# Kernel optimization log

Hardware: AMD Instinct MI355X
Metric: run time of the kernel (lower is better)

Reference implementation:

```python
import jax, jax.numpy as jnp
import numpy as np

NUM_HEADS = 8
NUM_KEY_FEATURES = 128  # 32*1 + 32*3 (key fiber num_features)
N_NODES = 50000
N_EDGES = 500000
CH = 32  # value/key channels per degree


def setup_inputs() -> dict:
    key = jax.random.key(0)
    ks = jax.random.split(key, 7)
    return {
        "key0": jax.random.normal(ks[0], (N_EDGES, CH, 1), jnp.float32),
        "key1": jax.random.normal(ks[1], (N_EDGES, CH, 3), jnp.float32),
        "value0": jax.random.normal(ks[2], (N_EDGES, CH, 1), jnp.float32),
        "value1": jax.random.normal(ks[3], (N_EDGES, CH, 3), jnp.float32),
        "query0": jax.random.normal(ks[4], (N_NODES, CH, 1), jnp.float32),
        "query1": jax.random.normal(ks[5], (N_NODES, CH, 3), jnp.float32),
        "dst": jax.random.randint(ks[6], (N_EDGES,), 0, N_NODES, jnp.int64),
    }


def _to_heads(d0, d1):
    # Fiber.to_attention_heads: per-degree [*, C, 2d+1] -> [*, H, C//H*(2d+1)], concat over degrees
    a = d0.reshape(d0.shape[0], NUM_HEADS, -1)
    b = d1.reshape(d1.shape[0], NUM_HEADS, -1)
    return jnp.concatenate([a, b], axis=-1)  # [*, H, 16]


def reference(key0, key1, value0, value1, query0, query1, dst):
    n_nodes = query0.shape[0]
    k = _to_heads(key0, key1)      # [E, H, F]
    q = _to_heads(query0, query1)  # [N, H, F]
    # dgl.ops.e_dot_v: dot(key_e, query_{dst(e)}) per head
    logits = jnp.einsum('ehf,ehf->eh', k, q[dst]) / np.sqrt(NUM_KEY_FEATURES).astype(np.float32)
    # edge_softmax over incoming edges of each dst node
    m = jax.ops.segment_max(logits, dst, num_segments=n_nodes)       # [N, H]
    ex = jnp.exp(logits - m[dst])                                    # [E, H]
    s = jax.ops.segment_sum(ex, dst, num_segments=n_nodes)          # [N, H]
    w = ex / s[dst]                                                  # [E, H]

    def agg(v):
        e, c, dd = v.shape
        vh = v.reshape(e, NUM_HEADS, c // NUM_HEADS, dd)
        wv = w[:, :, None, None] * vh                                # [E, H, C/H, 2d+1]
        out = jax.ops.segment_sum(wv, dst, num_segments=n_nodes)
        return out.reshape(n_nodes, c, dd)                           # [N, C, 2d+1]

    return agg(value0), agg(value1)
```

## Files before the change

kernel.cpp:

```cpp
#include <hip/hip_runtime.h>
#include <hip/hip_bf16.h>
#include <math.h>

#define NHEADS 8
#define CHVAL 32
#define SCB 1024
#define WPB 4

__global__ void logits_kernel(const float4* __restrict__ key0,
                              const float4* __restrict__ key1,
                              const float4* __restrict__ q0,
                              const float4* __restrict__ q1,
                              const int* __restrict__ dst,
                              float* __restrict__ logits,
                              int* __restrict__ cnt,
                              int EH) {
    int tid = blockIdx.x * blockDim.x + threadIdx.x;
    if (tid >= EH) return;
    int e = tid >> 3;
    int h = tid & 7;
    int n = dst[e];
    int qh = n * 8 + h;

    float4 a = key0[tid];
    float4 qa = q0[qh];
    float dot = a.x * qa.x + a.y * qa.y + a.z * qa.z + a.w * qa.w;
#pragma unroll
    for (int j = 0; j < 3; ++j) {
        float4 b  = key1[tid * 3 + j];
        float4 qb = q1[qh * 3 + j];
        dot += b.x * qb.x + b.y * qb.y + b.z * qb.z + b.w * qb.w;
    }
    logits[tid] = dot * 0.08838834764831845f;
    if (h == 0) atomicAdd(&cnt[n], 1);
}

__global__ void scan1_kernel(int* __restrict__ cnt, int* __restrict__ btot, int N) {
    __shared__ int sh[SCB];
    int t = threadIdx.x;
    int i = blockIdx.x * SCB + t;
    int v = (i < N) ? cnt[i] : 0;
    sh[t] = v;
    __syncthreads();
    for (int off = 1; off < SCB; off <<= 1) {
        int y = (t >= off) ? sh[t - off] : 0;
        __syncthreads();
        sh[t] += y;
        __syncthreads();
    }
    if (i < N) cnt[i] = sh[t] - v;
    if (t == SCB - 1) btot[blockIdx.x] = sh[t];
}

__global__ void scan2_kernel(int* __restrict__ btot, int nb) {
    __shared__ int sh[64];
    int t = threadIdx.x;
    int v = (t < nb) ? btot[t] : 0;
    sh[t] = v;
    __syncthreads();
    for (int off = 1; off < 64; off <<= 1) {
        int y = (t >= off) ? sh[t - off] : 0;
        __syncthreads();
        sh[t] += y;
        __syncthreads();
    }
    if (t < nb) btot[t] = sh[t] - v;
}

__global__ void scan3_kernel(const int* __restrict__ cnt, const int* __restrict__ btot,
                             int* __restrict__ offs, int* __restrict__ cursor,
                             int N, int E) {
    int i = blockIdx.x * blockDim.x + threadIdx.x;
    if (i < N) {
        int o = cnt[i] + btot[i >> 10];
        offs[i] = o;
        cursor[i] = o;
    }
    if (i == 0) offs[N] = E;
}

__global__ void scatter_kernel(const int* __restrict__ dst,
                               int* __restrict__ cursor,
                               int* __restrict__ eid,
                               int E) {
    int e = blockIdx.x * blockDim.x + threadIdx.x;
    if (e < E) {
        int pos = atomicAdd(&cursor[dst[e]], 1);
        eid[pos] = e;
    }
}

__global__ void __launch_bounds__(64 * WPB)
node_kernel(const float* __restrict__ logits,
            const float4* __restrict__ value0,
            const float4* __restrict__ value1,
            const int* __restrict__ offs,
            const int* __restrict__ eid,
            float4* __restrict__ out0,
            float4* __restrict__ out1,
            int N) {
    __shared__ float w_sh[WPB][64][9];

    int wv = threadIdx.x >> 6;
    int t  = threadIdx.x & 63;
    int n  = blockIdx.x * WPB + wv;
    if (n >= N) return;

    int beg = offs[n];
    int deg = offs[n + 1] - beg;

    if (deg == 0) {
        float4 z = {0.f, 0.f, 0.f, 0.f};
        if (t < 8) out0[(size_t)n * 8 + t] = z;
        else if (t < 32) out1[(size_t)n * 24 + (t - 8)] = z;
        return;
    }

    int myeid = -1;
    float lg[8];
    if (t < deg) {
        myeid = eid[beg + t];
        const float4* lp = (const float4*)(logits + (size_t)myeid * 8);
        float4 a = lp[0], b = lp[1];
        lg[0] = a.x; lg[1] = a.y; lg[2] = a.z; lg[3] = a.w;
        lg[4] = b.x; lg[5] = b.y; lg[6] = b.z; lg[7] = b.w;
    } else {
#pragma unroll
        for (int k = 0; k < 8; ++k) lg[k] = -INFINITY;
    }

    float mx[8];
#pragma unroll
    for (int k = 0; k < 8; ++k) mx[k] = lg[k];
    for (int base = 64; base < deg; base += 64) {
        if (base + t < deg) {
            int e = eid[beg + base + t];
            const float4* lp = (const float4*)(logits + (size_t)e * 8);
            float4 a = lp[0], b = lp[1];
            float tt[8] = {a.x, a.y, a.z, a.w, b.x, b.y, b.z, b.w};
#pragma unroll
            for (int k = 0; k < 8; ++k) mx[k] = fmaxf(mx[k], tt[k]);
        }
    }
#pragma unroll
    for (int k = 0; k < 8; ++k)
        for (int off = 32; off; off >>= 1)
            mx[k] = fmaxf(mx[k], __shfl_xor(mx[k], off, 64));

    float ex0[8], sm[8];
#pragma unroll
    for (int k = 0; k < 8; ++k) { ex0[k] = __expf(lg[k] - mx[k]); sm[k] = ex0[k]; }
    for (int base = 64; base < deg; base += 64) {
        if (base + t < deg) {
            int e = eid[beg + base + t];
            const float4* lp = (const float4*)(logits + (size_t)e * 8);
            float4 a = lp[0], b = lp[1];
            float tt[8] = {a.x, a.y, a.z, a.w, b.x, b.y, b.z, b.w};
#pragma unroll
            for (int k = 0; k < 8; ++k) sm[k] += __expf(tt[k] - mx[k]);
        }
    }
#pragma unroll
    for (int k = 0; k < 8; ++k)
        for (int off = 32; off; off >>= 1)
            sm[k] += __shfl_xor(sm[k], off, 64);
    float inv[8];
#pragma unroll
    for (int k = 0; k < 8; ++k) inv[k] = 1.0f / sm[k];

    int half = t >> 5;
    int l = t & 31;
    int myh = (l < 8) ? l : ((l - 8) / 3);
    float4 acc = {0.f, 0.f, 0.f, 0.f};

    for (int base = 0; base < deg; base += 64) {
        int clen = min(64, deg - base);
        if (base == 0) {
            if (t < clen) {
#pragma unroll
                for (int k = 0; k < 8; ++k) w_sh[wv][t][k] = ex0[k] * inv[k];
            }
        } else {
            if (base + t < deg) {
                int e = eid[beg + base + t];
                const float4* lp = (const float4*)(logits + (size_t)e * 8);
                float4 a = lp[0], b = lp[1];
                float tt[8] = {a.x, a.y, a.z, a.w, b.x, b.y, b.z, b.w};
#pragma unroll
                for (int k = 0; k < 8; ++k)
                    w_sh[wv][t][k] = __expf(tt[k] - mx[k]) * inv[k];
            }
        }
        __builtin_amdgcn_wave_barrier();

        for (int ii = half; ii < clen; ii += 2) {
            int e = (base == 0) ? __shfl(myeid, ii, 64)
                                : eid[beg + base + ii];
            float w = w_sh[wv][ii][myh];
            float4 v = (l < 8) ? value0[(size_t)e * 8 + l]
                               : value1[(size_t)e * 24 + (l - 8)];
            acc.x += w * v.x;
            acc.y += w * v.y;
            acc.z += w * v.z;
            acc.w += w * v.w;
        }
        __builtin_amdgcn_wave_barrier();
    }

    acc.x += __shfl_xor(acc.x, 32, 64);
    acc.y += __shfl_xor(acc.y, 32, 64);
    acc.z += __shfl_xor(acc.z, 32, 64);
    acc.w += __shfl_xor(acc.w, 32, 64);
    if (t < 8)       out0[(size_t)n * 8 + l] = acc;
    else if (t < 32) out1[(size_t)n * 24 + (l - 8)] = acc;
}

extern "C" void kernel_launch(void* const* d_in, const int* in_sizes, int n_in,
                              void* d_out, int out_size, void* d_ws, size_t ws_size,
                              hipStream_t stream) {
    const float* key0   = (const float*)d_in[0];
    const float* key1   = (const float*)d_in[1];
    const float* value0 = (const float*)d_in[2];
    const float* value1 = (const float*)d_in[3];
    const float* query0 = (const float*)d_in[4];
    const float* query1 = (const float*)d_in[5];
    const int*   dst    = (const int*)d_in[6];

    int E = in_sizes[0] / CHVAL;
    int N = in_sizes[4] / CHVAL;
    int EH = E * NHEADS;
    int nb = (N + SCB - 1) / SCB;

    float* logits = (float*)d_ws;
    int*   cnt    = (int*)(logits + EH);
    int*   offs   = cnt + N;
    int*   cursor = offs + N + 1;
    int*   eid    = cursor + N;
    int*   btot   = eid + E;

    float* out0 = (float*)d_out;
    float* out1 = out0 + (size_t)N * 32;

    hipMemsetAsync(cnt, 0, (size_t)N * sizeof(int), stream);

    int blk = 256;
    logits_kernel<<<(EH + blk - 1) / blk, blk, 0, stream>>>(
        (const float4*)key0, (const float4*)key1,
        (const float4*)query0, (const float4*)query1,
        dst, logits, cnt, EH);

    scan1_kernel<<<nb, SCB, 0, stream>>>(cnt, btot, N);
    scan2_kernel<<<1, 64, 0, stream>>>(btot, nb);
    scan3_kernel<<<(N + blk - 1) / blk, blk, 0, stream>>>(cnt, btot, offs, cursor, N, E);

    scatter_kernel<<<(E + blk - 1) / blk, blk, 0, stream>>>(dst, cursor, eid, E);

    int nnb = (N + WPB - 1) / WPB;
    node_kernel<<<nnb, 64 * WPB, 0, stream>>>(logits,
                                              (const float4*)value0,
                                              (const float4*)value1,
                                              offs, eid,
                                              (float4*)out0, (float4*)out1, N);
}
```

Baseline: 190.0 us.

## Fuse logit computation into node kernel, replacing logits pass with histogram

Removes the separate per-edge logits kernel and its logits buffer. Each node wave now computes key·query dot products for its incoming edges directly, with query loaded once per node. The first 64 logits stay in registers and edge ids are cached in shared memory. This avoids writing and re-reading the E×8 logits array and replaces the logits kernel with a simple histogram pass. Edges beyond the first 64 per node get their keys re-read and re-dotted up to three times, and the key gathers are now random-access by edge id rather than streamed.

```diff
diff --git a/kernel.cpp b/kernel.cpp
--- a/kernel.cpp
+++ b/kernel.cpp
@@ -7,32 +7,9 @@
 #define SCB 1024
 #define WPB 4
 
-__global__ void logits_kernel(const float4* __restrict__ key0,
-                              const float4* __restrict__ key1,
-                              const float4* __restrict__ q0,
-                              const float4* __restrict__ q1,
-                              const int* __restrict__ dst,
-                              float* __restrict__ logits,
-                              int* __restrict__ cnt,
-                              int EH) {
-    int tid = blockIdx.x * blockDim.x + threadIdx.x;
-    if (tid >= EH) return;
-    int e = tid >> 3;
-    int h = tid & 7;
-    int n = dst[e];
-    int qh = n * 8 + h;
-
-    float4 a = key0[tid];
-    float4 qa = q0[qh];
-    float dot = a.x * qa.x + a.y * qa.y + a.z * qa.z + a.w * qa.w;
-#pragma unroll
-    for (int j = 0; j < 3; ++j) {
-        float4 b  = key1[tid * 3 + j];
-        float4 qb = q1[qh * 3 + j];
-        dot += b.x * qb.x + b.y * qb.y + b.z * qb.z + b.w * qb.w;
-    }
-    logits[tid] = dot * 0.08838834764831845f;
-    if (h == 0) atomicAdd(&cnt[n], 1);
+__global__ void hist_kernel(const int* __restrict__ dst, int* __restrict__ cnt, int E) {
+    int e = blockIdx.x * blockDim.x + threadIdx.x;
+    if (e < E) atomicAdd(&cnt[dst[e]], 1);
 }
 
 __global__ void scan1_kernel(int* __restrict__ cnt, int* __restrict__ btot, int N) {
@@ -91,7 +68,10 @@
 }
 
 __global__ void __launch_bounds__(64 * WPB)
-node_kernel(const float* __restrict__ logits,
+node_kernel(const float4* __restrict__ key0,
+            const float4* __restrict__ key1,
+            const float4* __restrict__ q0,
+            const float4* __restrict__ q1,
             const float4* __restrict__ value0,
             const float4* __restrict__ value1,
             const int* __restrict__ offs,
@@ -100,6 +80,7 @@
             float4* __restrict__ out1,
             int N) {
     __shared__ float w_sh[WPB][64][9];
+    __shared__ int   e_sh[WPB][64];
 
     int wv = threadIdx.x >> 6;
     int t  = threadIdx.x & 63;
@@ -116,86 +97,99 @@
         return;
     }
 
-    int myeid = -1;
-    float lg[8];
-    if (t < deg) {
-        myeid = eid[beg + t];
-        const float4* lp = (const float4*)(logits + (size_t)myeid * 8);
-        float4 a = lp[0], b = lp[1];
-        lg[0] = a.x; lg[1] = a.y; lg[2] = a.z; lg[3] = a.w;
-        lg[4] = b.x; lg[5] = b.y; lg[6] = b.z; lg[7] = b.w;
-    } else {
+    const float SCALE = 0.08838834764831845f;
+    int s = t >> 3;
+    int h = t & 7;
+
+    float4 qa  = q0[(size_t)n * 8 + h];
+    float4 qb0 = q1[(size_t)n * 24 + 3 * h + 0];
+    float4 qb1 = q1[(size_t)n * 24 + 3 * h + 1];
+    float4 qb2 = q1[(size_t)n * 24 + 3 * h + 2];
+
+    auto compute_lg = [&](int slot, int& e_out) -> float {
+        int e = eid[beg + slot];
+        e_out = e;
+        float4 ka  = key0[(size_t)e * 8 + h];
+        float4 kb0 = key1[(size_t)e * 24 + 3 * h + 0];
+        float4 kb1 = key1[(size_t)e * 24 + 3 * h + 1];
+        float4 kb2 = key1[(size_t)e * 24 + 3 * h + 2];
+        float d = ka.x * qa.x + ka.y * qa.y + ka.z * qa.z + ka.w * qa.w
+                + kb0.x * qb0.x + kb0.y * qb0.y + kb0.z * qb0.z + kb0.w * qb0.w
+                + kb1.x * qb1.x + kb1.y * qb1.y + kb1.z * qb1.z + kb1.w * qb1.w
+                + kb2.x * qb2.x + kb2.y * qb2.y + kb2.z * qb2.z + kb2.w * qb2.w;
+        return d * SCALE;
+    };
+
+    float lgreg[8];
+    float mxl = -INFINITY;
 #pragma unroll
-        for (int k = 0; k < 8; ++k) lg[k] = -INFINITY;
-    }
-
-    float mx[8];
+    for (int r = 0; r < 8; ++r) {
+        int slot = r * 8 + s;
+        float lg = -INFINITY;
+        if (slot < deg) {
+            int e;
+            lg = compute_lg(slot, e);
+            if (h == 0) e_sh[wv][slot] = e;
+        }
+        lgreg[r] = lg;
+        mxl = fmaxf(mxl, lg);
+    }
+    for (int slot = 64 + s; slot < deg; slot += 8) {
+        int e;
+        mxl = fmaxf(mxl, compute_lg(slot, e));
+    }
+    mxl = fmaxf(mxl, __shfl_xor(mxl, 8, 64));
+    mxl = fmaxf(mxl, __shfl_xor(mxl, 16, 64));
+    mxl = fmaxf(mxl, __shfl_xor(mxl, 32, 64));
+
+    float sml = 0.0f;
 #pragma unroll
-    for (int k = 0; k < 8; ++k) mx[k] = lg[k];
-    for (int base = 64; base < deg; base += 64) {
-        if (base + t < deg) {
-            int e = eid[beg + base + t];
-            const float4* lp = (const float4*)(logits + (size_t)e * 8);
-            float4 a = lp[0], b = lp[1];
-            float tt[8] = {a.x, a.y, a.z, a.w, b.x, b.y, b.z, b.w};
+    for (int r = 0; r < 8; ++r) sml += __expf(lgreg[r] - mxl);
+    for (int slot = 64 + s; slot < deg; slot += 8) {
+        int e;
+        sml += __expf(compute_lg(slot, e) - mxl);
+    }
+    sml += __shfl_xor(sml, 8, 64);
+    sml += __shfl_xor(sml, 16, 64);
+    sml += __shfl_xor(sml, 32, 64);
+    float inv = 1.0f / sml;
+
 #pragma unroll
-            for (int k = 0; k < 8; ++k) mx[k] = fmaxf(mx[k], tt[k]);
-        }
-    }
-#pragma unroll
-    for (int k = 0; k < 8; ++k)
-        for (int off = 32; off; off >>= 1)
-            mx[k] = fmaxf(mx[k], __shfl_xor(mx[k], off, 64));
-
-    float ex0[8], sm[8];
-#pragma unroll
-    for (int k = 0; k < 8; ++k) { ex0[k] = __expf(lg[k] - mx[k]); sm[k] = ex0[k]; }
-    for (int base = 64; base < deg; base += 64) {
-        if (base + t < deg) {
-            int e = eid[beg + base + t];
-            const float4* lp = (const float4*)(logits + (size_t)e * 8);
-            float4 a = lp[0], b = lp[1];
-            float tt[8] = {a.x, a.y, a.z, a.w, b.x, b.y, b.z, b.w};
-#pragma unroll
-            for (int k = 0; k < 8; ++k) sm[k] += __expf(tt[k] - mx[k]);
-        }
-    }
-#pragma unroll
-    for (int k = 0; k < 8; ++k)
-        for (int off = 32; off; off >>= 1)
-            sm[k] += __shfl_xor(sm[k], off, 64);
-    float inv[8];
-#pragma unroll
-    for (int k = 0; k < 8; ++k) inv[k] = 1.0f / sm[k];
+    for (int r = 0; r < 8; ++r) {
+        int slot = r * 8 + s;
+        if (slot < deg) w_sh[wv][slot][h] = __expf(lgreg[r] - mxl) * inv;
+    }
+    __builtin_amdgcn_wave_barrier();
 
     int half = t >> 5;
     int l = t & 31;
     int myh = (l < 8) ? l : ((l - 8) / 3);
     float4 acc = {0.f, 0.f, 0.f, 0.f};
 
-    for (int base = 0; base < deg; base += 64) {
+    int clen0 = min(deg, 64);
+    for (int ii = half; ii < clen0; ii += 2) {
+        int e = e_sh[wv][ii];
+        float w = w_sh[wv][ii][myh];
+        float4 v = (l < 8) ? value0[(size_t)e * 8 + l]
+                           : value1[(size_t)e * 24 + (l - 8)];
+        acc.x += w * v.x;
+        acc.y += w * v.y;
+        acc.z += w * v.z;
+        acc.w += w * v.w;
+    }
+
+    for (int base = 64; base < deg; base += 64) {
+        __builtin_amdgcn_wave_barrier();
         int clen = min(64, deg - base);
-        if (base == 0) {
-            if (t < clen) {
-#pragma unroll
-                for (int k = 0; k < 8; ++k) w_sh[wv][t][k] = ex0[k] * inv[k];
-            }
-        } else {
-            if (base + t < deg) {
-                int e = eid[beg + base + t];
-                const float4* lp = (const float4*)(logits + (size_t)e * 8);
-                float4 a = lp[0], b = lp[1];
-                float tt[8] = {a.x, a.y, a.z, a.w, b.x, b.y, b.z, b.w};
-#pragma unroll
-                for (int k = 0; k < 8; ++k)
-                    w_sh[wv][t][k] = __expf(tt[k] - mx[k]) * inv[k];
-            }
+        for (int loc = s; loc < clen; loc += 8) {
+            int e;
+            float lg = compute_lg(base + loc, e);
+            if (h == 0) e_sh[wv][loc] = e;
+            w_sh[wv][loc][h] = __expf(lg - mxl) * inv;
         }
         __builtin_amdgcn_wave_barrier();
-
         for (int ii = half; ii < clen; ii += 2) {
-            int e = (base == 0) ? __shfl(myeid, ii, 64)
-                                : eid[beg + base + ii];
+            int e = e_sh[wv][ii];
             float w = w_sh[wv][ii][myh];
             float4 v = (l < 8) ? value0[(size_t)e * 8 + l]
                                : value1[(size_t)e * 24 + (l - 8)];
@@ -204,7 +198,6 @@
             acc.z += w * v.z;
             acc.w += w * v.w;
         }
-        __builtin_amdgcn_wave_barrier();
     }
 
     acc.x += __shfl_xor(acc.x, 32, 64);
@@ -228,15 +221,13 @@
 
     int E = in_sizes[0] / CHVAL;
     int N = in_sizes[4] / CHVAL;
-    int EH = E * NHEADS;
     int nb = (N + SCB - 1) / SCB;
 
-    float* logits = (float*)d_ws;
-    int*   cnt    = (int*)(logits + EH);
-    int*   offs   = cnt + N;
-    int*   cursor = offs + N + 1;
-    int*   eid    = cursor + N;
-    int*   btot   = eid + E;
+    int* cnt    = (int*)d_ws;
+    int* offs   = cnt + N;
+    int* cursor = offs + N + 1;
+    int* eid    = cursor + N;
+    int* btot   = eid + E;
 
     float* out0 = (float*)d_out;
     float* out1 = out0 + (size_t)N * 32;
@@ -244,10 +235,7 @@
     hipMemsetAsync(cnt, 0, (size_t)N * sizeof(int), stream);
 
     int blk = 256;
-    logits_kernel<<<(EH + blk - 1) / blk, blk, 0, stream>>>(
-        (const float4*)key0, (const float4*)key1,
-        (const float4*)query0, (const float4*)query1,
-        dst, logits, cnt, EH);
+    hist_kernel<<<(E + blk - 1) / blk, blk, 0, stream>>>(dst, cnt, E);
 
     scan1_kernel<<<nb, SCB, 0, stream>>>(cnt, btot, N);
     scan2_kernel<<<1, 64, 0, stream>>>(btot, nb);
@@ -256,9 +244,10 @@
     scatter_kernel<<<(E + blk - 1) / blk, blk, 0, stream>>>(dst, cursor, eid, E);
 
     int nnb = (N + WPB - 1) / WPB;
-    node_kernel<<<nnb, 64 * WPB, 0, stream>>>(logits,
-                                              (const float4*)value0,
-                                              (const float4*)value1,
-                                              offs, eid,
-                                              (float4*)out0, (float4*)out1, N);
-}
+    node_kernel<<<nnb, 64 * WPB, 0, stream>>>(
+        (const float4*)key0, (const float4*)key1,
+        (const float4*)query0, (const float4*)query1,
+        (const float4*)value0, (const float4*)value1,
+        offs, eid,
+        (float4*)out0, (float4*)out1, N);
+}
```

New measurement: 307.3 us. +61.8%, slower.

## Compute logits in CSR order after sorting edges by destination

Applied to the files above, without the earlier changes.

Edge logits are now computed after the CSR build. Each thread walks edges in destination-sorted order and writes logits contiguously by CSR position, so the node kernel reads logits sequentially instead of gathering them through eid. A separate histogram kernel replaces the fused atomic count, and the scatter also records the node id for each CSR slot. In exchange, key loads in the logits kernel become gathers through eid, and there is one extra pass over dst plus an extra nid array.

```diff
diff --git a/kernel.cpp b/kernel.cpp
--- a/kernel.cpp
+++ b/kernel.cpp
@@ -7,32 +7,9 @@
 #define SCB 1024
 #define WPB 4
 
-__global__ void logits_kernel(const float4* __restrict__ key0,
-                              const float4* __restrict__ key1,
-                              const float4* __restrict__ q0,
-                              const float4* __restrict__ q1,
-                              const int* __restrict__ dst,
-                              float* __restrict__ logits,
-                              int* __restrict__ cnt,
-                              int EH) {
-    int tid = blockIdx.x * blockDim.x + threadIdx.x;
-    if (tid >= EH) return;
-    int e = tid >> 3;
-    int h = tid & 7;
-    int n = dst[e];
-    int qh = n * 8 + h;
-
-    float4 a = key0[tid];
-    float4 qa = q0[qh];
-    float dot = a.x * qa.x + a.y * qa.y + a.z * qa.z + a.w * qa.w;
-#pragma unroll
-    for (int j = 0; j < 3; ++j) {
-        float4 b  = key1[tid * 3 + j];
-        float4 qb = q1[qh * 3 + j];
-        dot += b.x * qb.x + b.y * qb.y + b.z * qb.z + b.w * qb.w;
-    }
-    logits[tid] = dot * 0.08838834764831845f;
-    if (h == 0) atomicAdd(&cnt[n], 1);
+__global__ void hist_kernel(const int* __restrict__ dst, int* __restrict__ cnt, int E) {
+    int e = blockIdx.x * blockDim.x + threadIdx.x;
+    if (e < E) atomicAdd(&cnt[dst[e]], 1);
 }
 
 __global__ void scan1_kernel(int* __restrict__ cnt, int* __restrict__ btot, int N) {
@@ -82,12 +59,44 @@
 __global__ void scatter_kernel(const int* __restrict__ dst,
                                int* __restrict__ cursor,
                                int* __restrict__ eid,
+                               int* __restrict__ nid,
                                int E) {
     int e = blockIdx.x * blockDim.x + threadIdx.x;
     if (e < E) {
-        int pos = atomicAdd(&cursor[dst[e]], 1);
+        int n = dst[e];
+        int pos = atomicAdd(&cursor[n], 1);
         eid[pos] = e;
-    }
+        nid[pos] = n;
+    }
+}
+
+__global__ void logits_csr_kernel(const float4* __restrict__ key0,
+                                  const float4* __restrict__ key1,
+                                  const float4* __restrict__ q0,
+                                  const float4* __restrict__ q1,
+                                  const int* __restrict__ eid,
+                                  const int* __restrict__ nid,
+                                  float* __restrict__ logits,
+                                  int EH) {
+    int tid = blockIdx.x * blockDim.x + threadIdx.x;
+    if (tid >= EH) return;
+    int pos = tid >> 3;
+    int h = tid & 7;
+    int e = eid[pos];
+    int n = nid[pos];
+    int kh = e * 8 + h;
+    int qh = n * 8 + h;
+
+    float4 a = key0[kh];
+    float4 qa = q0[qh];
+    float dot = a.x * qa.x + a.y * qa.y + a.z * qa.z + a.w * qa.w;
+#pragma unroll
+    for (int j = 0; j < 3; ++j) {
+        float4 b  = key1[kh * 3 + j];
+        float4 qb = q1[qh * 3 + j];
+        dot += b.x * qb.x + b.y * qb.y + b.z * qb.z + b.w * qb.w;
+    }
+    logits[tid] = dot * 0.08838834764831845f;
 }
 
 __global__ void __launch_bounds__(64 * WPB)
@@ -120,7 +129,7 @@
     float lg[8];
     if (t < deg) {
         myeid = eid[beg + t];
-        const float4* lp = (const float4*)(logits + (size_t)myeid * 8);
+        const float4* lp = (const float4*)(logits + (size_t)(beg + t) * 8);
         float4 a = lp[0], b = lp[1];
         lg[0] = a.x; lg[1] = a.y; lg[2] = a.z; lg[3] = a.w;
         lg[4] = b.x; lg[5] = b.y; lg[6] = b.z; lg[7] = b.w;
@@ -134,8 +143,7 @@
     for (int k = 0; k < 8; ++k) mx[k] = lg[k];
     for (int base = 64; base < deg; base += 64) {
         if (base + t < deg) {
-            int e = eid[beg + base + t];
-            const float4* lp = (const float4*)(logits + (size_t)e * 8);
+            const float4* lp = (const float4*)(logits + (size_t)(beg + base + t) * 8);
             float4 a = lp[0], b = lp[1];
             float tt[8] = {a.x, a.y, a.z, a.w, b.x, b.y, b.z, b.w};
 #pragma unroll
@@ -152,8 +160,7 @@
     for (int k = 0; k < 8; ++k) { ex0[k] = __expf(lg[k] - mx[k]); sm[k] = ex0[k]; }
     for (int base = 64; base < deg; base += 64) {
         if (base + t < deg) {
-            int e = eid[beg + base + t];
-            const float4* lp = (const float4*)(logits + (size_t)e * 8);
+            const float4* lp = (const float4*)(logits + (size_t)(beg + base + t) * 8);
             float4 a = lp[0], b = lp[1];
             float tt[8] = {a.x, a.y, a.z, a.w, b.x, b.y, b.z, b.w};
 #pragma unroll
@@ -182,8 +189,7 @@
             }
         } else {
             if (base + t < deg) {
-                int e = eid[beg + base + t];
-                const float4* lp = (const float4*)(logits + (size_t)e * 8);
+                const float4* lp = (const float4*)(logits + (size_t)(beg + base + t) * 8);
                 float4 a = lp[0], b = lp[1];
                 float tt[8] = {a.x, a.y, a.z, a.w, b.x, b.y, b.z, b.w};
 #pragma unroll
@@ -236,7 +242,8 @@
     int*   offs   = cnt + N;
     int*   cursor = offs + N + 1;
     int*   eid    = cursor + N;
-    int*   btot   = eid + E;
+    int*   nid    = eid + E;
+    int*   btot   = nid + E;
 
     float* out0 = (float*)d_out;
     float* out1 = out0 + (size_t)N * 32;
@@ -244,16 +251,18 @@
     hipMemsetAsync(cnt, 0, (size_t)N * sizeof(int), stream);
 
     int blk = 256;
-    logits_kernel<<<(EH + blk - 1) / blk, blk, 0, stream>>>(
-        (const float4*)key0, (const float4*)key1,
-        (const float4*)query0, (const float4*)query1,
-        dst, logits, cnt, EH);
+    hist_kernel<<<(E + blk - 1) / blk, blk, 0, stream>>>(dst, cnt, E);
 
     scan1_kernel<<<nb, SCB, 0, stream>>>(cnt, btot, N);
     scan2_kernel<<<1, 64, 0, stream>>>(btot, nb);
     scan3_kernel<<<(N + blk - 1) / blk, blk, 0, stream>>>(cnt, btot, offs, cursor, N, E);
 
-    scatter_kernel<<<(E + blk - 1) / blk, blk, 0, stream>>>(dst, cursor, eid, E);
+    scatter_kernel<<<(E + blk - 1) / blk, blk, 0, stream>>>(dst, cursor, eid, nid, E);
+
+    logits_csr_kernel<<<(EH + blk - 1) / blk, blk, 0, stream>>>(
+        (const float4*)key0, (const float4*)key1,
+        (const float4*)query0, (const float4*)query1,
+        eid, nid, logits, EH);
 
     int nnb = (N + WPB - 1) / WPB;
     node_kernel<<<nnb, 64 * WPB, 0, stream>>>(logits,
```

Measured after the change: 200.6 us. 5.6% more time.
